# Kernel tuning notes

Measured on AMD Instinct MI355X. Metric: run time of the kernel, lower is better.

The kernel has to match this reference:

```python
import jax, jax.numpy as jnp
import numpy as np

B, S, H, R, N = 8, 4096, 1024, 128, 256
A_LOGIT_INIT = 6.906754778648554      # logit(0.999)
DELTA_LOG_INIT = 0.5413248546129181   # log(exp(1.0) - 1.0), softplus^-1(1.0)


def setup_inputs() -> dict:
    key = jax.random.key(0)
    ks = jax.random.split(key, 6)
    x = jax.random.normal(ks[0], (B, S, H), dtype=jnp.float32)
    state0 = jnp.zeros((B, N), dtype=jnp.float32)
    in_basis = jax.random.normal(ks[1], (R, H), dtype=jnp.float32) / np.sqrt(H)
    q_select = jax.random.normal(ks[2], (N, R), dtype=jnp.float32) / np.sqrt(R)
    k_select = jax.random.normal(ks[3], (N, R), dtype=jnp.float32) / np.sqrt(R)
    v_input = jax.random.normal(ks[4], (N, R), dtype=jnp.float32) / np.sqrt(R)
    out_proj = jax.random.normal(ks[5], (H, N), dtype=jnp.float32) / np.sqrt(N)
    a_logit = jnp.full((N,), A_LOGIT_INIT, dtype=jnp.float32)
    delta_log = jnp.full((N,), DELTA_LOG_INIT, dtype=jnp.float32)
    return {"x": x, "state0": state0, "in_basis": in_basis, "q_select": q_select,
            "k_select": k_select, "v_input": v_input, "out_proj": out_proj,
            "a_logit": a_logit, "delta_log": delta_log}


def reference(x, state0, in_basis, q_select, k_select, v_input, out_proj,
              a_logit, delta_log):
    # Projections (all timesteps at once; equivalent to per-step F.linear)
    z = jnp.einsum('bsh,rh->bsr', x, in_basis)          # [B,S,R]
    b = jnp.einsum('bsr,nr->bsn', z, k_select)          # [B,S,N]
    c = jnp.einsum('bsr,nr->bsn', z, q_select)          # [B,S,N]
    v = jnp.einsum('bsr,nr->bsn', z, v_input)           # [B,S,N]

    a = jax.nn.sigmoid(a_logit)                         # [N]
    delta = jax.nn.softplus(delta_log)                  # [N]
    u = delta * (b * v)                                 # [B,S,N] driving input

    # Diagonal linear recurrence: s_t = a * s_{t-1} + u_t ; y_t = c_t * s_t
    u_t = jnp.swapaxes(u, 0, 1)                         # [S,B,N]
    c_t = jnp.swapaxes(c, 0, 1)                         # [S,B,N]

    def step(s, inp):
        u_i, c_i = inp
        s = a * s + u_i
        return s, c_i * s

    final_state, ys = jax.lax.scan(step, state0, (u_t, c_t))  # ys: [S,B,N]
    out = jnp.einsum('sbn,hn->bsh', ys, out_proj)       # [B,S,H]
    return out, final_state
```

## Files before the change

kernel.cpp:

```cpp
#include <hip/hip_runtime.h>
#include <math.h>

#define Bb 8
#define Ss 4096
#define Hh 1024
#define Rr 128
#define Nn 256
#define Mm (Bb*Ss)
#define LCH 128
#define NCHK (Ss/LCH)

typedef __attribute__((ext_vector_type(8))) short bf16x8;
typedef __attribute__((ext_vector_type(4))) float f32x4;

__device__ __forceinline__ float sigmoidf_(float x) { return 1.0f / (1.0f + expf(-x)); }
__device__ __forceinline__ float softplusf_(float x) { return log1pf(expf(x)); }

__device__ __forceinline__ unsigned short f2b(float f) {
    union { float f; unsigned int u; } v; v.f = f;
    return (unsigned short)((v.u + 0x7fffu + ((v.u >> 16) & 1u)) >> 16);
}
__device__ __forceinline__ float b2f(unsigned short h) {
    union { unsigned int u; float f; } v; v.u = ((unsigned int)h) << 16;
    return v.f;
}

__device__ __forceinline__ void gl_lds16(const void* g, void* l) {
    __builtin_amdgcn_global_load_lds(
        (const __attribute__((address_space(1))) void*)g,
        (__attribute__((address_space(3))) void*)l, 16, 0, 0);
}


__global__ __launch_bounds__(256)
void cast_w(const float* __restrict__ s0, const float* __restrict__ s1,
            const float* __restrict__ s2, const float* __restrict__ s3,
            const float* __restrict__ s4,
            unsigned short* __restrict__ d0, unsigned short* __restrict__ d1,
            unsigned short* __restrict__ d2, unsigned short* __restrict__ d3,
            unsigned short* __restrict__ d4)
{
    const int i = blockIdx.x * 256 + threadIdx.x;
    if (i < 131072)      d0[i] = f2b(s0[i]);
    else if (i < 163840) d1[i - 131072] = f2b(s1[i - 131072]);
    else if (i < 196608) d2[i - 163840] = f2b(s2[i - 163840]);
    else if (i < 229376) d3[i - 196608] = f2b(s3[i - 196608]);
    else                 d4[i - 229376] = f2b(s4[i - 229376]);
}

__global__ __launch_bounds__(256)
void g1_fused(const float* __restrict__ X, const unsigned short* __restrict__ IB,
              unsigned short* __restrict__ Z)
{
    __shared__ __align__(16) unsigned short As[64 * 32];
    __shared__ __align__(16) unsigned short Bs[128 * 32];
    const int tid = threadIdx.x;
    const int wave = tid >> 6, lane = tid & 63;
    const int m0 = blockIdx.x * 64;
    const int wm = (wave & 1) * 32, wn = (wave >> 1) * 64;
    const int quad = lane >> 4, lm = lane & 15;
    const int srow = lane >> 2;
    const int skoff = (((lane & 3) ^ ((srow >> 1) & 3)) << 3);
    const int qsw = ((quad ^ ((lm >> 1) & 3)) << 3);
    const int arow = tid >> 3;
    const int akf = (tid & 7) * 4;
    const int awoff = ((((tid & 7) >> 1) ^ ((arow >> 1) & 3)) << 3) + (tid & 1) * 4;

    f32x4 acc[2][4] = {};

    for (int k0 = 0; k0 < Hh; k0 += 32) {
#pragma unroll
        for (int q = 0; q < 2; ++q) {
            const int row = q * 32 + arow;
            const float4 v = *(const float4*)(X + (size_t)(m0 + row) * Hh + k0 + akf);
            uint2 o;
            o.x = (unsigned)f2b(v.x) | ((unsigned)f2b(v.y) << 16);
            o.y = (unsigned)f2b(v.z) | ((unsigned)f2b(v.w) << 16);
            *(uint2*)&As[row * 32 + awoff] = o;
        }
        gl_lds16(IB + (size_t)(2 * wave * 16 + srow) * Hh + k0 + skoff, &Bs[wave * 1024]);
        gl_lds16(IB + (size_t)((2 * wave + 1) * 16 + srow) * Hh + k0 + skoff, &Bs[wave * 1024 + 512]);
        __syncthreads();
        bf16x8 af[2], bfv[4];
#pragma unroll
        for (int i = 0; i < 2; ++i)
            af[i] = *(const bf16x8*)&As[(wm + i * 16 + lm) * 32 + qsw];
#pragma unroll
        for (int j = 0; j < 4; ++j)
            bfv[j] = *(const bf16x8*)&Bs[(wn + j * 16 + lm) * 32 + qsw];
#pragma unroll
        for (int i = 0; i < 2; ++i)
#pragma unroll
            for (int j = 0; j < 4; ++j)
                acc[i][j] = __builtin_amdgcn_mfma_f32_16x16x32_bf16(af[i], bfv[j], acc[i][j], 0, 0, 0);
        __syncthreads();
    }

#pragma unroll
    for (int i = 0; i < 2; ++i) {
        const int rbase = m0 + wm + i * 16 + quad * 4;
#pragma unroll
        for (int j = 0; j < 4; ++j) {
            const int col = wn + j * 16 + lm;
#pragma unroll
            for (int r = 0; r < 4; ++r)
                Z[(size_t)(rbase + r) * Rr + col] = f2b(acc[i][j][r]);
        }
    }
}

__global__ __launch_bounds__(256)
void proj_mfma(const unsigned short* __restrict__ Zm, const unsigned short* __restrict__ Kw,
               const unsigned short* __restrict__ Qw, const unsigned short* __restrict__ Vw,
               const float* __restrict__ delta_log, const float* __restrict__ a_logit,
               unsigned short* __restrict__ U, unsigned short* __restrict__ C,
               float* __restrict__ Pout)
{
    __shared__ __align__(16) char smem[34816];
    unsigned short* zs = (unsigned short*)smem;
    unsigned short* ks = (unsigned short*)(smem + 8192);
    unsigned short* qs = (unsigned short*)(smem + 12288);
    unsigned short* vs = (unsigned short*)(smem + 16384);
    float* uL = (float*)smem;
    float* pcomb = (float*)(smem + 33792);

    const int tid = threadIdx.x;
    const int wave = tid >> 6, lane = tid & 63;
    const int m0 = blockIdx.x * 128, n0 = blockIdx.y * 64;
    const int wm = (wave & 1) * 64, wn = (wave >> 1) * 32;
    const int quad = lane >> 4, lm = lane & 15;
    const int srow = lane >> 2;
    const int skoff = (((lane & 3) ^ ((srow >> 1) & 3)) << 3);
    const int qsw = ((quad ^ ((lm >> 1) & 3)) << 3);

    f32x4 aB[4][2] = {}, aC[4][2] = {}, aV[4][2] = {};

    for (int k0 = 0; k0 < Rr; k0 += 32) {
        gl_lds16(Zm + (size_t)(m0 + 2 * wave * 16 + srow) * Rr + k0 + skoff, &zs[wave * 1024]);
        gl_lds16(Zm + (size_t)(m0 + (2 * wave + 1) * 16 + srow) * Rr + k0 + skoff, &zs[wave * 1024 + 512]);
        gl_lds16(Kw + (size_t)(n0 + wave * 16 + srow) * Rr + k0 + skoff, &ks[wave * 512]);
        gl_lds16(Qw + (size_t)(n0 + wave * 16 + srow) * Rr + k0 + skoff, &qs[wave * 512]);
        gl_lds16(Vw + (size_t)(n0 + wave * 16 + srow) * Rr + k0 + skoff, &vs[wave * 512]);
        __syncthreads();
        bf16x8 zf[4], wf[2];
#pragma unroll
        for (int i = 0; i < 4; ++i)
            zf[i] = *(const bf16x8*)&zs[(wm + i * 16 + lm) * 32 + qsw];
#pragma unroll
        for (int j = 0; j < 2; ++j)
            wf[j] = *(const bf16x8*)&ks[(wn + j * 16 + lm) * 32 + qsw];
#pragma unroll
        for (int i = 0; i < 4; ++i)
#pragma unroll
            for (int j = 0; j < 2; ++j)
                aB[i][j] = __builtin_amdgcn_mfma_f32_16x16x32_bf16(zf[i], wf[j], aB[i][j], 0, 0, 0);
#pragma unroll
        for (int j = 0; j < 2; ++j)
            wf[j] = *(const bf16x8*)&qs[(wn + j * 16 + lm) * 32 + qsw];
#pragma unroll
        for (int i = 0; i < 4; ++i)
#pragma unroll
            for (int j = 0; j < 2; ++j)
                aC[i][j] = __builtin_amdgcn_mfma_f32_16x16x32_bf16(zf[i], wf[j], aC[i][j], 0, 0, 0);
#pragma unroll
        for (int j = 0; j < 2; ++j)
            wf[j] = *(const bf16x8*)&vs[(wn + j * 16 + lm) * 32 + qsw];
#pragma unroll
        for (int i = 0; i < 4; ++i)
#pragma unroll
            for (int j = 0; j < 2; ++j)
                aV[i][j] = __builtin_amdgcn_mfma_f32_16x16x32_bf16(zf[i], wf[j], aV[i][j], 0, 0, 0);
        __syncthreads();
    }

    float dl[2];
#pragma unroll
    for (int j = 0; j < 2; ++j)
        dl[j] = softplusf_(delta_log[n0 + wn + j * 16 + lm]);

#pragma unroll
    for (int i = 0; i < 4; ++i) {
        const int lrow = wm + i * 16 + quad * 4;
        const int rbase = m0 + lrow;
#pragma unroll
        for (int j = 0; j < 2; ++j) {
            const int col = wn + j * 16 + lm;
            const int gcol = n0 + col;
#pragma unroll
            for (int r = 0; r < 4; ++r) {
                const float uval = dl[j] * aB[i][j][r] * aV[i][j][r];
                const size_t idx = (size_t)(rbase + r) * Nn + gcol;
                U[idx] = f2b(uval);
                C[idx] = f2b(aC[i][j][r]);
                uL[(lrow + r) * 66 + col] = uval;
            }
        }
    }
    __syncthreads();

    const int colp = tid & 63, seg = tid >> 6;
    const float a = sigmoidf_(a_logit[n0 + colp]);
    float l = 0.0f;
#pragma unroll 8
    for (int r = 0; r < 32; ++r)
        l = fmaf(a, l, uL[(seg * 32 + r) * 66 + colp]);
    pcomb[seg * 64 + colp] = l;
    __syncthreads();
    if (tid < 64) {
        float a32 = a;
#pragma unroll
        for (int i = 0; i < 5; ++i) a32 *= a32;
        const float Pv = ((pcomb[tid] * a32 + pcomb[64 + tid]) * a32
                          + pcomb[128 + tid]) * a32 + pcomb[192 + tid];
        Pout[(size_t)blockIdx.x * Nn + n0 + tid] = Pv;
    }
}

__global__ __launch_bounds__(256)
void scan_mid(const float* __restrict__ P, const float* __restrict__ state0,
              const float* __restrict__ a_logit,
              float* __restrict__ start, float* __restrict__ final_state)
{
    const int g = blockIdx.x * blockDim.x + threadIdx.x;
    const int n = g & (Nn - 1);
    const int b = g >> 8;
    const float a = sigmoidf_(a_logit[n]);
    float aL = a;
#pragma unroll
    for (int i = 0; i < 7; ++i) aL *= aL;
    float s = state0[g];
#pragma unroll
    for (int ch = 0; ch < NCHK; ++ch) {
        const size_t idx = ((size_t)(b * NCHK + ch)) * Nn + n;
        start[idx] = s;
        s = fmaf(aL, s, P[idx]);
    }
    final_state[g] = s;
}

__global__ __launch_bounds__(256)
void scan_chunk_c(unsigned short* __restrict__ uy, const unsigned short* __restrict__ cm,
                  const float* __restrict__ start, const float* __restrict__ a_logit)
{
    const int g = blockIdx.x * blockDim.x + threadIdx.x;
    const int n = g & (Nn - 1);
    const int rest = g >> 8;
    const int ch = rest & (NCHK - 1);
    const int b = rest >> 5;
    const float a = sigmoidf_(a_logit[n]);
    float s = start[((size_t)(b * NCHK + ch)) * Nn + n];
    size_t idx = ((size_t)(b * Ss + ch * LCH)) * Nn + n;
#pragma unroll 8
    for (int t = 0; t < LCH; ++t) {
        s = fmaf(a, s, b2f(uy[idx]));
        uy[idx] = f2b(b2f(cm[idx]) * s);
        idx += Nn;
    }
}

__global__ __launch_bounds__(256)
void mfma_nt_f32(const unsigned short* __restrict__ A, const unsigned short* __restrict__ B,
                 float* __restrict__ Cout, int M, int N, int K)
{
    __shared__ __align__(16) unsigned short As[128 * 32];
    __shared__ __align__(16) unsigned short Bs[128 * 32];
    const int tid = threadIdx.x;
    const int wave = tid >> 6, lane = tid & 63;
    const int m0 = blockIdx.x * 128, n0 = blockIdx.y * 128;
    const int wm = (wave & 1) * 64, wn = (wave >> 1) * 64;
    const int quad = lane >> 4, lm = lane & 15;
    const int srow = lane >> 2;
    const int skoff = (((lane & 3) ^ ((srow >> 1) & 3)) << 3);
    const int qsw = ((quad ^ ((lm >> 1) & 3)) << 3);
    const int r0 = wave * 2, r1 = r0 + 1;

    f32x4 acc[4][4] = {};

    for (int k0 = 0; k0 < K; k0 += 32) {
        gl_lds16(A + (size_t)(m0 + r0 * 16 + srow) * K + k0 + skoff, &As[r0 * 512]);
        gl_lds16(A + (size_t)(m0 + r1 * 16 + srow) * K + k0 + skoff, &As[r1 * 512]);
        gl_lds16(B + (size_t)(n0 + r0 * 16 + srow) * K + k0 + skoff, &Bs[r0 * 512]);
        gl_lds16(B + (size_t)(n0 + r1 * 16 + srow) * K + k0 + skoff, &Bs[r1 * 512]);
        __syncthreads();
        bf16x8 af[4], bfv[4];
#pragma unroll
        for (int i = 0; i < 4; ++i)
            af[i] = *(const bf16x8*)&As[(wm + i * 16 + lm) * 32 + qsw];
#pragma unroll
        for (int j = 0; j < 4; ++j)
            bfv[j] = *(const bf16x8*)&Bs[(wn + j * 16 + lm) * 32 + qsw];
#pragma unroll
        for (int i = 0; i < 4; ++i)
#pragma unroll
            for (int j = 0; j < 4; ++j)
                acc[i][j] = __builtin_amdgcn_mfma_f32_16x16x32_bf16(af[i], bfv[j], acc[i][j], 0, 0, 0);
        __syncthreads();
    }

#pragma unroll
    for (int i = 0; i < 4; ++i) {
        const int rbase = m0 + wm + i * 16 + quad * 4;
#pragma unroll
        for (int j = 0; j < 4; ++j) {
            const int col = n0 + wn + j * 16 + lm;
#pragma unroll
            for (int r = 0; r < 4; ++r)
                Cout[(size_t)(rbase + r) * N + col] = acc[i][j][r];
        }
    }
}

extern "C" void kernel_launch(void* const* d_in, const int* in_sizes, int n_in,
                              void* d_out, int out_size, void* d_ws, size_t ws_size,
                              hipStream_t stream)
{
    const float* x         = (const float*)d_in[0];
    const float* state0    = (const float*)d_in[1];
    const float* in_basis  = (const float*)d_in[2];
    const float* q_select  = (const float*)d_in[3];
    const float* k_select  = (const float*)d_in[4];
    const float* v_input   = (const float*)d_in[5];
    const float* out_proj  = (const float*)d_in[6];
    const float* a_logit   = (const float*)d_in[7];
    const float* delta_log = (const float*)d_in[8];

    float* out = (float*)d_out;
    float* final_state = out + (size_t)Mm * Hh;

    char* ws = (char*)d_ws;
    unsigned short* u  = (unsigned short*)ws;
    unsigned short* c  = (unsigned short*)(ws + 16777216);
    unsigned short* zb = (unsigned short*)(ws + 33554432);
    unsigned short* ib = (unsigned short*)(ws + 41943040);
    unsigned short* kb = (unsigned short*)(ws + 42205184);
    unsigned short* qb = (unsigned short*)(ws + 42270720);
    unsigned short* vb = (unsigned short*)(ws + 42336256);
    unsigned short* ob = (unsigned short*)(ws + 42401792);
    float* P  = (float*)(ws + 42926080);
    float* st = (float*)(ws + 43188224);

    cast_w<<<491520 / 256, 256, 0, stream>>>(in_basis, k_select, q_select, v_input, out_proj,
                                             ib, kb, qb, vb, ob);

    g1_fused<<<Mm / 64, 256, 0, stream>>>(x, ib, zb);

    proj_mfma<<<dim3(Mm / 128, Nn / 64), 256, 0, stream>>>(zb, kb, qb, vb,
                                                           delta_log, a_logit, u, c, P);

    scan_mid<<<(Bb * Nn) / 256, 256, 0, stream>>>(P, state0, a_logit, st, final_state);
    scan_chunk_c<<<(Bb * NCHK * Nn) / 256, 256, 0, stream>>>(u, c, st, a_logit);

    mfma_nt_f32<<<dim3(Mm / 128, Hh / 128), 256, 0, stream>>>(u, ob, out, Mm, Hh, Nn);
}
```

Baseline: 323.0 us.

## Double-buffer LDS tiles in the three MFMA GEMM kernels

Adds a second LDS buffer to g1_fused, proj_mfma and mfma_nt_f32. Each kernel now issues the global loads for the next K-slice before running the MFMAs on the current slice, leaving one barrier per iteration. The goal is to hide global-load latency behind compute. In exchange, LDS use per block roughly doubles, which may lower occupancy, and the extra live registers may add pressure.

```diff
diff --git a/kernel.cpp b/kernel.cpp
--- a/kernel.cpp
+++ b/kernel.cpp
@@ -52,8 +52,8 @@
 void g1_fused(const float* __restrict__ X, const unsigned short* __restrict__ IB,
               unsigned short* __restrict__ Z)
 {
-    __shared__ __align__(16) unsigned short As[64 * 32];
-    __shared__ __align__(16) unsigned short Bs[128 * 32];
+    __shared__ __align__(16) unsigned short As[2][64 * 32];
+    __shared__ __align__(16) unsigned short Bs[2][128 * 32];
     const int tid = threadIdx.x;
     const int wave = tid >> 6, lane = tid & 63;
     const int m0 = blockIdx.x * 64;
@@ -67,33 +67,56 @@
     const int awoff = ((((tid & 7) >> 1) ^ ((arow >> 1) & 3)) << 3) + (tid & 1) * 4;
 
     f32x4 acc[2][4] = {};
-
+    float4 va[2];
+
+#pragma unroll
+    for (int q = 0; q < 2; ++q)
+        va[q] = *(const float4*)(X + (size_t)(m0 + q * 32 + arow) * Hh + akf);
+    gl_lds16(IB + (size_t)(2 * wave * 16 + srow) * Hh + skoff, &Bs[0][wave * 1024]);
+    gl_lds16(IB + (size_t)((2 * wave + 1) * 16 + srow) * Hh + skoff, &Bs[0][wave * 1024 + 512]);
+#pragma unroll
+    for (int q = 0; q < 2; ++q) {
+        uint2 o;
+        o.x = (unsigned)f2b(va[q].x) | ((unsigned)f2b(va[q].y) << 16);
+        o.y = (unsigned)f2b(va[q].z) | ((unsigned)f2b(va[q].w) << 16);
+        *(uint2*)&As[0][(q * 32 + arow) * 32 + awoff] = o;
+    }
+    __syncthreads();
+
+    int cur = 0;
     for (int k0 = 0; k0 < Hh; k0 += 32) {
-#pragma unroll
-        for (int q = 0; q < 2; ++q) {
-            const int row = q * 32 + arow;
-            const float4 v = *(const float4*)(X + (size_t)(m0 + row) * Hh + k0 + akf);
-            uint2 o;
-            o.x = (unsigned)f2b(v.x) | ((unsigned)f2b(v.y) << 16);
-            o.y = (unsigned)f2b(v.z) | ((unsigned)f2b(v.w) << 16);
-            *(uint2*)&As[row * 32 + awoff] = o;
-        }
-        gl_lds16(IB + (size_t)(2 * wave * 16 + srow) * Hh + k0 + skoff, &Bs[wave * 1024]);
-        gl_lds16(IB + (size_t)((2 * wave + 1) * 16 + srow) * Hh + k0 + skoff, &Bs[wave * 1024 + 512]);
-        __syncthreads();
+        const int nxt = cur ^ 1;
+        const bool more = (k0 + 32) < Hh;
+        if (more) {
+            gl_lds16(IB + (size_t)(2 * wave * 16 + srow) * Hh + k0 + 32 + skoff, &Bs[nxt][wave * 1024]);
+            gl_lds16(IB + (size_t)((2 * wave + 1) * 16 + srow) * Hh + k0 + 32 + skoff, &Bs[nxt][wave * 1024 + 512]);
+#pragma unroll
+            for (int q = 0; q < 2; ++q)
+                va[q] = *(const float4*)(X + (size_t)(m0 + q * 32 + arow) * Hh + k0 + 32 + akf);
+        }
         bf16x8 af[2], bfv[4];
 #pragma unroll
         for (int i = 0; i < 2; ++i)
-            af[i] = *(const bf16x8*)&As[(wm + i * 16 + lm) * 32 + qsw];
+            af[i] = *(const bf16x8*)&As[cur][(wm + i * 16 + lm) * 32 + qsw];
 #pragma unroll
         for (int j = 0; j < 4; ++j)
-            bfv[j] = *(const bf16x8*)&Bs[(wn + j * 16 + lm) * 32 + qsw];
+            bfv[j] = *(const bf16x8*)&Bs[cur][(wn + j * 16 + lm) * 32 + qsw];
 #pragma unroll
         for (int i = 0; i < 2; ++i)
 #pragma unroll
             for (int j = 0; j < 4; ++j)
                 acc[i][j] = __builtin_amdgcn_mfma_f32_16x16x32_bf16(af[i], bfv[j], acc[i][j], 0, 0, 0);
+        if (more) {
+#pragma unroll
+            for (int q = 0; q < 2; ++q) {
+                uint2 o;
+                o.x = (unsigned)f2b(va[q].x) | ((unsigned)f2b(va[q].y) << 16);
+                o.y = (unsigned)f2b(va[q].z) | ((unsigned)f2b(va[q].w) << 16);
+                *(uint2*)&As[nxt][(q * 32 + arow) * 32 + awoff] = o;
+            }
+        }
         __syncthreads();
+        cur = nxt;
     }
 
 #pragma unroll
@@ -107,6 +130,22 @@
                 Z[(size_t)(rbase + r) * Rr + col] = f2b(acc[i][j][r]);
         }
     }
+}
+
+__device__ __forceinline__ void proj_stage(const unsigned short* Zm, const unsigned short* Kw,
+                                           const unsigned short* Qw, const unsigned short* Vw,
+                                           char* bb, int m0, int n0, int k0,
+                                           int wave, int srow, int skoff)
+{
+    unsigned short* zs = (unsigned short*)bb;
+    unsigned short* ks = (unsigned short*)(bb + 8192);
+    unsigned short* qs = (unsigned short*)(bb + 12288);
+    unsigned short* vs = (unsigned short*)(bb + 16384);
+    gl_lds16(Zm + (size_t)(m0 + 2 * wave * 16 + srow) * Rr + k0 + skoff, &zs[wave * 1024]);
+    gl_lds16(Zm + (size_t)(m0 + (2 * wave + 1) * 16 + srow) * Rr + k0 + skoff, &zs[wave * 1024 + 512]);
+    gl_lds16(Kw + (size_t)(n0 + wave * 16 + srow) * Rr + k0 + skoff, &ks[wave * 512]);
+    gl_lds16(Qw + (size_t)(n0 + wave * 16 + srow) * Rr + k0 + skoff, &qs[wave * 512]);
+    gl_lds16(Vw + (size_t)(n0 + wave * 16 + srow) * Rr + k0 + skoff, &vs[wave * 512]);
 }
 
 __global__ __launch_bounds__(256)
@@ -116,13 +155,9 @@
                unsigned short* __restrict__ U, unsigned short* __restrict__ C,
                float* __restrict__ Pout)
 {
-    __shared__ __align__(16) char smem[34816];
-    unsigned short* zs = (unsigned short*)smem;
-    unsigned short* ks = (unsigned short*)(smem + 8192);
-    unsigned short* qs = (unsigned short*)(smem + 12288);
-    unsigned short* vs = (unsigned short*)(smem + 16384);
+    __shared__ __align__(16) char smem[41984];
     float* uL = (float*)smem;
-    float* pcomb = (float*)(smem + 33792);
+    float* pcomb = (float*)(smem + 40960);
 
     const int tid = threadIdx.x;
     const int wave = tid >> 6, lane = tid & 63;
@@ -135,20 +170,25 @@
 
     f32x4 aB[4][2] = {}, aC[4][2] = {}, aV[4][2] = {};
 
-    for (int k0 = 0; k0 < Rr; k0 += 32) {
-        gl_lds16(Zm + (size_t)(m0 + 2 * wave * 16 + srow) * Rr + k0 + skoff, &zs[wave * 1024]);
-        gl_lds16(Zm + (size_t)(m0 + (2 * wave + 1) * 16 + srow) * Rr + k0 + skoff, &zs[wave * 1024 + 512]);
-        gl_lds16(Kw + (size_t)(n0 + wave * 16 + srow) * Rr + k0 + skoff, &ks[wave * 512]);
-        gl_lds16(Qw + (size_t)(n0 + wave * 16 + srow) * Rr + k0 + skoff, &qs[wave * 512]);
-        gl_lds16(Vw + (size_t)(n0 + wave * 16 + srow) * Rr + k0 + skoff, &vs[wave * 512]);
-        __syncthreads();
+    proj_stage(Zm, Kw, Qw, Vw, smem, m0, n0, 0, wave, srow, skoff);
+    __syncthreads();
+
+    int cur = 0;
+    for (int p = 0; p < 4; ++p) {
+        if (p < 3)
+            proj_stage(Zm, Kw, Qw, Vw, smem + (cur ^ 1) * 20480, m0, n0,
+                       (p + 1) * 32, wave, srow, skoff);
+        const unsigned short* zsc = (const unsigned short*)(smem + cur * 20480);
+        const unsigned short* ksc = zsc + 4096;
+        const unsigned short* qsc = zsc + 6144;
+        const unsigned short* vsc = zsc + 8192;
         bf16x8 zf[4], wf[2];
 #pragma unroll
         for (int i = 0; i < 4; ++i)
-            zf[i] = *(const bf16x8*)&zs[(wm + i * 16 + lm) * 32 + qsw];
+            zf[i] = *(const bf16x8*)&zsc[(wm + i * 16 + lm) * 32 + qsw];
 #pragma unroll
         for (int j = 0; j < 2; ++j)
-            wf[j] = *(const bf16x8*)&ks[(wn + j * 16 + lm) * 32 + qsw];
+            wf[j] = *(const bf16x8*)&ksc[(wn + j * 16 + lm) * 32 + qsw];
 #pragma unroll
         for (int i = 0; i < 4; ++i)
 #pragma unroll
@@ -156,7 +196,7 @@
                 aB[i][j] = __builtin_amdgcn_mfma_f32_16x16x32_bf16(zf[i], wf[j], aB[i][j], 0, 0, 0);
 #pragma unroll
         for (int j = 0; j < 2; ++j)
-            wf[j] = *(const bf16x8*)&qs[(wn + j * 16 + lm) * 32 + qsw];
+            wf[j] = *(const bf16x8*)&qsc[(wn + j * 16 + lm) * 32 + qsw];
 #pragma unroll
         for (int i = 0; i < 4; ++i)
 #pragma unroll
@@ -164,13 +204,14 @@
                 aC[i][j] = __builtin_amdgcn_mfma_f32_16x16x32_bf16(zf[i], wf[j], aC[i][j], 0, 0, 0);
 #pragma unroll
         for (int j = 0; j < 2; ++j)
-            wf[j] = *(const bf16x8*)&vs[(wn + j * 16 + lm) * 32 + qsw];
+            wf[j] = *(const bf16x8*)&vsc[(wn + j * 16 + lm) * 32 + qsw];
 #pragma unroll
         for (int i = 0; i < 4; ++i)
 #pragma unroll
             for (int j = 0; j < 2; ++j)
                 aV[i][j] = __builtin_amdgcn_mfma_f32_16x16x32_bf16(zf[i], wf[j], aV[i][j], 0, 0, 0);
         __syncthreads();
+        cur ^= 1;
     }
 
     float dl[2];
@@ -262,8 +303,8 @@
 void mfma_nt_f32(const unsigned short* __restrict__ A, const unsigned short* __restrict__ B,
                  float* __restrict__ Cout, int M, int N, int K)
 {
-    __shared__ __align__(16) unsigned short As[128 * 32];
-    __shared__ __align__(16) unsigned short Bs[128 * 32];
+    __shared__ __align__(16) unsigned short As[2][128 * 32];
+    __shared__ __align__(16) unsigned short Bs[2][128 * 32];
     const int tid = threadIdx.x;
     const int wave = tid >> 6, lane = tid & 63;
     const int m0 = blockIdx.x * 128, n0 = blockIdx.y * 128;
@@ -276,25 +317,35 @@
 
     f32x4 acc[4][4] = {};
 
+    gl_lds16(A + (size_t)(m0 + r0 * 16 + srow) * K + skoff, &As[0][r0 * 512]);
+    gl_lds16(A + (size_t)(m0 + r1 * 16 + srow) * K + skoff, &As[0][r1 * 512]);
+    gl_lds16(B + (size_t)(n0 + r0 * 16 + srow) * K + skoff, &Bs[0][r0 * 512]);
+    gl_lds16(B + (size_t)(n0 + r1 * 16 + srow) * K + skoff, &Bs[0][r1 * 512]);
+    __syncthreads();
+
+    int cur = 0;
     for (int k0 = 0; k0 < K; k0 += 32) {
-        gl_lds16(A + (size_t)(m0 + r0 * 16 + srow) * K + k0 + skoff, &As[r0 * 512]);
-        gl_lds16(A + (size_t)(m0 + r1 * 16 + srow) * K + k0 + skoff, &As[r1 * 512]);
-        gl_lds16(B + (size_t)(n0 + r0 * 16 + srow) * K + k0 + skoff, &Bs[r0 * 512]);
-        gl_lds16(B + (size_t)(n0 + r1 * 16 + srow) * K + k0 + skoff, &Bs[r1 * 512]);
-        __syncthreads();
+        const int nxt = cur ^ 1;
+        if (k0 + 32 < K) {
+            gl_lds16(A + (size_t)(m0 + r0 * 16 + srow) * K + k0 + 32 + skoff, &As[nxt][r0 * 512]);
+            gl_lds16(A + (size_t)(m0 + r1 * 16 + srow) * K + k0 + 32 + skoff, &As[nxt][r1 * 512]);
+            gl_lds16(B + (size_t)(n0 + r0 * 16 + srow) * K + k0 + 32 + skoff, &Bs[nxt][r0 * 512]);
+            gl_lds16(B + (size_t)(n0 + r1 * 16 + srow) * K + k0 + 32 + skoff, &Bs[nxt][r1 * 512]);
+        }
         bf16x8 af[4], bfv[4];
 #pragma unroll
         for (int i = 0; i < 4; ++i)
-            af[i] = *(const bf16x8*)&As[(wm + i * 16 + lm) * 32 + qsw];
+            af[i] = *(const bf16x8*)&As[cur][(wm + i * 16 + lm) * 32 + qsw];
 #pragma unroll
         for (int j = 0; j < 4; ++j)
-            bfv[j] = *(const bf16x8*)&Bs[(wn + j * 16 + lm) * 32 + qsw];
+            bfv[j] = *(const bf16x8*)&Bs[cur][(wn + j * 16 + lm) * 32 + qsw];
 #pragma unroll
         for (int i = 0; i < 4; ++i)
 #pragma unroll
             for (int j = 0; j < 4; ++j)
                 acc[i][j] = __builtin_amdgcn_mfma_f32_16x16x32_bf16(af[i], bfv[j], acc[i][j], 0, 0, 0);
         __syncthreads();
+        cur = nxt;
     }
 
 #pragma unroll
```

Result: no change. 318.8 us (-1.3%).
